# Kernel tuning notes

Measured on AMD Instinct MI355X. Metric: run time of the kernel, lower is better.

## Reference

```python
import jax, jax.numpy as jnp
import numpy as np

DECAY_EPS = 1e-8  # matches F.cosine_similarity eps
DECAY_RATE = 0.999  # buffer decay_rate


def setup_inputs() -> dict:
    key = jax.random.key(0)
    ks = jax.random.split(key, 6)
    B, M, D = 256, 65536, 1024
    return {
        "query": jax.random.normal(ks[0], (B, D), dtype=jnp.float32),
        "mem_keys": jax.random.normal(ks[1], (M, D), dtype=jnp.float32),
        "mem_values": jax.random.normal(ks[2], (M, D), dtype=jnp.float32),
        "importance": jax.random.uniform(ks[3], (M,), dtype=jnp.float32),
        "access_times": jax.random.randint(ks[4], (M,), 0, 1000, dtype=jnp.int32),
        "access_counts": jax.random.randint(ks[5], (M,), 1, 50, dtype=jnp.int32),
        "current_time": 1000,
        "top_k": 8,
    }


def reference(query, mem_keys, mem_values, importance, access_times, access_counts, current_time, top_k):
    # Batched version of AdaptiveMemoryBuffer.retrieve.
    # query: [B, D]; mem_keys/mem_values: [M, D]; importance/access_*: [M]
    qn = query / jnp.maximum(jnp.linalg.norm(query, axis=-1, keepdims=True), DECAY_EPS)
    kn = mem_keys / jnp.maximum(jnp.linalg.norm(mem_keys, axis=-1, keepdims=True), DECAY_EPS)
    sim = qn @ kn.T  # [B, M] cosine similarity

    dt = (current_time - access_times).astype(jnp.float32)           # time since access
    retention = jnp.power(jnp.float32(DECAY_RATE), dt)               # forgetting curve
    freq_bonus = jnp.log1p(access_counts.astype(jnp.float32))        # log(1 + count)
    scores = sim * (retention * importance * freq_bonus)[None, :]    # [B, M]

    top_scores, top_idx = jax.lax.top_k(scores, top_k)                # [B, k]
    weights = jax.nn.softmax(top_scores, axis=-1)                     # [B, k]
    combined = jnp.einsum('bk,bkd->bd', weights, mem_values[top_idx]) # weighted gather
    confidence = weights.max(axis=-1)                                 # [B]
    return combined, confidence
```

## Files before the change

kernel.cpp:

```cpp
#include <hip/hip_runtime.h>
#include <math.h>
#include <float.h>

typedef __attribute__((ext_vector_type(8))) short short8;
typedef __attribute__((ext_vector_type(8))) ushort ushort8;
typedef __attribute__((ext_vector_type(4))) float f32x4;

namespace {

constexpr int B = 256;
constexpr int M = 65536;
constexpr int D = 1024;
constexpr float DECAY_EPS = 1e-8f;
constexpr float DECAY_RATE = 0.999f;

constexpr int BN = 32;
constexpr int BK = 32;
constexpr int KSTEPS = D / BK;

constexpr int CHUNKS = 8;
constexpr int CHUNK = M / CHUNKS;
constexpr int NCAND = CHUNKS * 8;

__device__ inline ushort f2bf(float f) {
  union { float f; unsigned u; } v; v.f = f;
  unsigned r = v.u + 0x7fffu + ((v.u >> 16) & 1u);
  return (ushort)(r >> 16);
}

__global__ void prep_q_kernel(const float* __restrict__ q, ushort* __restrict__ qnf) {
  const int r = blockIdx.x;
  const int t = threadIdx.x;
  float4 v = reinterpret_cast<const float4*>(q + (size_t)r * D)[t];
  float ss = v.x * v.x + v.y * v.y + v.z * v.z + v.w * v.w;
#pragma unroll
  for (int off = 32; off; off >>= 1) ss += __shfl_down(ss, off, 64);
  __shared__ float red[4];
  if ((t & 63) == 0) red[t >> 6] = ss;
  __syncthreads();
  const float inv = 1.0f / fmaxf(sqrtf(red[0] + red[1] + red[2] + red[3]), DECAY_EPS);
  ushort4 o;
  o.x = f2bf(v.x * inv); o.y = f2bf(v.y * inv);
  o.z = f2bf(v.z * inv); o.w = f2bf(v.w * inv);
  const int k0 = t * 4;
  const int kt = k0 >> 5;
  const int lane_slot = (r & 15) + 16 * ((k0 & 31) >> 3);
  const int j0 = k0 & 7;
  *reinterpret_cast<ushort4*>(qnf + (size_t)(kt * 16 + (r >> 4)) * 512 + lane_slot * 8 + j0) = o;
}

__global__ __launch_bounds__(512, 8) void score_gemm_kernel(
    const ushort* __restrict__ qnf, const float* __restrict__ keys,
    const float* __restrict__ importance, const int* __restrict__ atimes,
    const int* __restrict__ acnts, const int* __restrict__ ctime,
    ushort* __restrict__ scores) {
  __shared__ alignas(16) ushort Bs[2][BN * BK];
  __shared__ float cscale[BN];

  const int t = threadIdx.x;
  const int lane = t & 63;
  const int w = t >> 6;
  const int h = lane >> 4;
  const int q = lane & 15;
  const int jb = blockIdx.x * BN;

  const int rw = t >> 4;
  const int cw = t & 15;
  const float2* kp2 = reinterpret_cast<const float2*>(keys + (size_t)(jb + rw) * D) + cw;
  const int wo = rw * BK + (((cw >> 2) ^ ((rw >> 1) & 3)) * 4 + (cw & 3)) * 2;

  int roff[2];
#pragma unroll
  for (int nf = 0; nf < 2; ++nf) {
    const int row = nf * 16 + q;
    roff[nf] = row * BK + ((h ^ ((row >> 1) & 3)) * 8);
  }

  f32x4 acc[2][2];
#pragma unroll
  for (int f = 0; f < 2; ++f)
#pragma unroll
    for (int n = 0; n < 2; ++n) acc[f][n] = (f32x4)(0.0f);

  float kn2 = 0.0f;
  float2 nv;

  nv = kp2[0];
  kn2 += nv.x * nv.x + nv.y * nv.y;
  *reinterpret_cast<uint*>(&Bs[0][wo]) = (uint)f2bf(nv.x) | ((uint)f2bf(nv.y) << 16);
  nv = kp2[16];
  __syncthreads();

  const short8* apbase = reinterpret_cast<const short8*>(qnf);

  for (int s = 0; s < KSTEPS; ++s) {
    const int cur = s & 1;
    short8 a0 = apbase[(size_t)(s * 16 + 2 * w + 0) * 64 + lane];
    short8 a1 = apbase[(size_t)(s * 16 + 2 * w + 1) * 64 + lane];
    short8 b0 = *reinterpret_cast<const short8*>(&Bs[cur][roff[0]]);
    short8 b1 = *reinterpret_cast<const short8*>(&Bs[cur][roff[1]]);
    acc[0][0] = __builtin_amdgcn_mfma_f32_16x16x32_bf16(a0, b0, acc[0][0], 0, 0, 0);
    acc[0][1] = __builtin_amdgcn_mfma_f32_16x16x32_bf16(a0, b1, acc[0][1], 0, 0, 0);
    acc[1][0] = __builtin_amdgcn_mfma_f32_16x16x32_bf16(a1, b0, acc[1][0], 0, 0, 0);
    acc[1][1] = __builtin_amdgcn_mfma_f32_16x16x32_bf16(a1, b1, acc[1][1], 0, 0, 0);
    if (s + 1 < KSTEPS) {
      kn2 += nv.x * nv.x + nv.y * nv.y;
      *reinterpret_cast<uint*>(&Bs[cur ^ 1][wo]) =
          (uint)f2bf(nv.x) | ((uint)f2bf(nv.y) << 16);
      if (s + 2 < KSTEPS) nv = kp2[(s + 2) * 16];
    }
    __syncthreads();
  }

  kn2 += __shfl_xor(kn2, 1, 64);
  kn2 += __shfl_xor(kn2, 2, 64);
  kn2 += __shfl_xor(kn2, 4, 64);
  kn2 += __shfl_xor(kn2, 8, 64);
  if (q == 0) {
    const int j = jb + rw;
    const float dt = (float)(ctime[0] - atimes[j]);
    const float mult = powf(DECAY_RATE, dt) * importance[j] * log1pf((float)acnts[j]);
    cscale[rw] = mult / fmaxf(sqrtf(kn2), DECAY_EPS);
  }
  __syncthreads();

#pragma unroll
  for (int f = 0; f < 2; ++f) {
    const int row0 = (2 * w + f) * 16 + (h << 2);
#pragma unroll
    for (int nf = 0; nf < 2; ++nf) {
      const float cs = cscale[nf * 16 + q];
#pragma unroll
      for (int rr = 0; rr < 4; ++rr) {
        const float v = acc[f][nf][rr] * cs;
        const float vn = __shfl_xor(v, 1, 64);
        if (!(q & 1)) {
          const uint pk = (uint)f2bf(v) | ((uint)f2bf(vn) << 16);
          *reinterpret_cast<uint*>(
              scores + (size_t)(row0 + rr) * M + jb + nf * 16 + q) = pk;
        }
      }
    }
  }
}

__global__ __launch_bounds__(256) void topk_partial_kernel(
    const ushort* __restrict__ scores, int* __restrict__ cand_i) {
  const int b = blockIdx.y;
  const int c = blockIdx.x;
  const int t = threadIdx.x;
  const int lane = t & 63, w = t >> 6;
  const ushort8* base8 =
      reinterpret_cast<const ushort8*>(scores + (size_t)b * M + (size_t)c * CHUNK);

  uint s8[8];
#pragma unroll
  for (int i = 0; i < 8; ++i) s8[i] = 0;

  auto ins = [&](uint x) {
    if (x > s8[0]) {
#pragma unroll
      for (int i = 0; i < 8; ++i) {
        const bool up = (i < 7) && (x > s8[i + 1]);
        const uint keep = (x > s8[i]) ? x : s8[i];
        s8[i] = up ? s8[i + 1] : keep;
      }
    }
  };

  const uint jbase = (uint)c * CHUNK;
#pragma unroll
  for (int it = 0; it < CHUNK / (256 * 8); ++it) {
    const int slot = it * 256 + t;
    const ushort8 v = base8[slot];
    const uint j0 = jbase + (uint)slot * 8;
#pragma unroll
    for (int e = 0; e < 8; ++e) {
      const ushort s = (ushort)v[e];
      const ushort key = (s & 0x8000) ? (ushort)~s : (ushort)(s | 0x8000);
      ins(((uint)key << 16) | ((j0 + e) & 0xFFFFu));
    }
  }

  __shared__ uint ls[2048];
#pragma unroll
  for (int i = 0; i < 8; ++i) ls[t * 8 + i] = s8[i];
  __syncthreads();

  __shared__ uint rs4[4];
  __shared__ int rp4[4];
  for (int r = 0; r < 8; ++r) {
    uint ms = 0;
    int mp = 0;
#pragma unroll
    for (int i = 0; i < 8; ++i) {
      const uint v = ls[i * 256 + t];
      if (v > ms) { ms = v; mp = i * 256 + t; }
    }
#pragma unroll
    for (int off = 32; off; off >>= 1) {
      const uint ov = __shfl_xor(ms, off, 64);
      const int op = __shfl_xor(mp, off, 64);
      if (ov > ms) { ms = ov; mp = op; }
    }
    if (lane == 0) { rs4[w] = ms; rp4[w] = mp; }
    __syncthreads();
    if (t == 0) {
      uint bs = 0;
      int bp = 0;
#pragma unroll
      for (int i = 0; i < 4; ++i)
        if (rs4[i] > bs) { bs = rs4[i]; bp = rp4[i]; }
      cand_i[((size_t)b * CHUNKS + c) * 8 + r] = (int)(ls[bp] & 0xFFFFu);
      ls[bp] = 0;
    }
    __syncthreads();
  }
}

__global__ __launch_bounds__(512) void rescore_kernel(
    const int* __restrict__ cand_i, const float* __restrict__ query,
    const float* __restrict__ keys, const float* __restrict__ values,
    const float* __restrict__ importance, const int* __restrict__ atimes,
    const int* __restrict__ acnts, const int* __restrict__ ctime,
    float* __restrict__ outc, float* __restrict__ conf) {
  const int b = blockIdx.x;
  const int t = threadIdx.x;
  const int lane = t & 63, w = t >> 6;

  const float4* qv4 = reinterpret_cast<const float4*>(query + (size_t)b * D + lane * 16);
  float4 q0 = qv4[0], q1 = qv4[1], q2 = qv4[2], q3 = qv4[3];
  float ssq = q0.x * q0.x + q0.y * q0.y + q0.z * q0.z + q0.w * q0.w
            + q1.x * q1.x + q1.y * q1.y + q1.z * q1.z + q1.w * q1.w
            + q2.x * q2.x + q2.y * q2.y + q2.z * q2.z + q2.w * q2.w
            + q3.x * q3.x + q3.y * q3.y + q3.z * q3.z + q3.w * q3.w;
#pragma unroll
  for (int off = 32; off; off >>= 1) ssq += __shfl_xor(ssq, off, 64);
  const float qdn = fmaxf(sqrtf(ssq), DECAY_EPS);
  const int ct = ctime[0];

  __shared__ float sc[NCAND];
  __shared__ int sidx[NCAND];

  for (int u = 0; u < 8; ++u) {
    const int c = w * 8 + u;
    const int j = cand_i[(size_t)b * NCAND + c];
    const float4* kv4 = reinterpret_cast<const float4*>(keys + (size_t)j * D + lane * 16);
    const float4 k0 = kv4[0], k1 = kv4[1], k2 = kv4[2], k3 = kv4[3];
    float dd = q0.x * k0.x + q0.y * k0.y + q0.z * k0.z + q0.w * k0.w
             + q1.x * k1.x + q1.y * k1.y + q1.z * k1.z + q1.w * k1.w
             + q2.x * k2.x + q2.y * k2.y + q2.z * k2.z + q2.w * k2.w
             + q3.x * k3.x + q3.y * k3.y + q3.z * k3.z + q3.w * k3.w;
    float nn = k0.x * k0.x + k0.y * k0.y + k0.z * k0.z + k0.w * k0.w
             + k1.x * k1.x + k1.y * k1.y + k1.z * k1.z + k1.w * k1.w
             + k2.x * k2.x + k2.y * k2.y + k2.z * k2.z + k2.w * k2.w
             + k3.x * k3.x + k3.y * k3.y + k3.z * k3.z + k3.w * k3.w;
#pragma unroll
    for (int off = 32; off; off >>= 1) {
      dd += __shfl_xor(dd, off, 64);
      nn += __shfl_xor(nn, off, 64);
    }
    if (lane == 0) {
      const float dtv = (float)(ct - atimes[j]);
      const float mult = powf(DECAY_RATE, dtv) * importance[j] * log1pf((float)acnts[j]);
      sc[c] = dd / (qdn * fmaxf(sqrtf(nn), DECAY_EPS)) * mult;
      sidx[c] = j;
    }
  }
  __syncthreads();

  __shared__ float w8s[8];
  __shared__ int g8[8];
  __shared__ float confv;
  __shared__ float tls[8];
  __shared__ int tli[8];
  if (w == 0) {
    float myv = sc[lane];
    for (int r = 0; r < 8; ++r) {
      float m = myv;
      int mi = lane;
#pragma unroll
      for (int off = 32; off; off >>= 1) {
        const float ov = __shfl_xor(m, off, 64);
        const int oi = __shfl_xor(mi, off, 64);
        if (ov > m || (ov == m && oi < mi)) { m = ov; mi = oi; }
      }
      if (lane == 0) { tls[r] = m; tli[r] = mi; }
      if (lane == mi) myv = -FLT_MAX;
    }
    if (lane == 0) {
      const float mx = tls[0];
      float e[8];
      float z = 0.0f;
#pragma unroll
      for (int r = 0; r < 8; ++r) { e[r] = expf(tls[r] - mx); z += e[r]; }
      const float invz = 1.0f / z;
#pragma unroll
      for (int r = 0; r < 8; ++r) { w8s[r] = e[r] * invz; g8[r] = sidx[tli[r]]; }
      confv = w8s[0];
    }
  }
  __syncthreads();

  float2 acc = make_float2(0.0f, 0.0f);
#pragma unroll
  for (int k = 0; k < 8; ++k) {
    const float wk = w8s[k];
    const float2 v = *reinterpret_cast<const float2*>(values + (size_t)g8[k] * D + 2 * t);
    acc.x = fmaf(wk, v.x, acc.x);
    acc.y = fmaf(wk, v.y, acc.y);
  }
  *reinterpret_cast<float2*>(outc + (size_t)b * D + 2 * t) = acc;
  if (t == 0) conf[b] = confv;
}

}

extern "C" void kernel_launch(void* const* d_in, const int* in_sizes, int n_in,
                              void* d_out, int out_size, void* d_ws, size_t ws_size,
                              hipStream_t stream) {
  const float* query = (const float*)d_in[0];
  const float* keys = (const float*)d_in[1];
  const float* values = (const float*)d_in[2];
  const float* importance = (const float*)d_in[3];
  const int* atimes = (const int*)d_in[4];
  const int* acnts = (const int*)d_in[5];
  const int* ctime = (const int*)d_in[6];

  float* out = (float*)d_out;
  ushort* qnf = (ushort*)d_ws;
  ushort* scores = qnf + (size_t)B * D;
  int* cand = (int*)(scores + (size_t)B * M);

  prep_q_kernel<<<B, 256, 0, stream>>>(query, qnf);
  score_gemm_kernel<<<M / BN, 512, 0, stream>>>(qnf, keys, importance, atimes,
                                                acnts, ctime, scores);
  dim3 gA(CHUNKS, B);
  topk_partial_kernel<<<gA, 256, 0, stream>>>(scores, cand);
  rescore_kernel<<<B, 512, 0, stream>>>(cand, query, keys, values, importance,
                                        atimes, acnts, ctime, out, out + (size_t)B * D);
}
```

Before: 163.6 us.

## Load key fragments directly into registers and drop LDS staging in score GEMM

```diff
diff --git a/kernel.cpp b/kernel.cpp
--- a/kernel.cpp
+++ b/kernel.cpp
@@ -1,4 +1,5 @@
 #include <hip/hip_runtime.h>
+#include <hip/hip_bf16.h>
 #include <math.h>
 #include <float.h>
 
@@ -15,8 +16,7 @@
 constexpr float DECAY_RATE = 0.999f;
 
 constexpr int BN = 32;
-constexpr int BK = 32;
-constexpr int KSTEPS = D / BK;
+constexpr int KSTEPS = D / 32;
 
 constexpr int CHUNKS = 8;
 constexpr int CHUNK = M / CHUNKS;
@@ -26,6 +26,22 @@
   union { float f; unsigned u; } v; v.f = f;
   unsigned r = v.u + 0x7fffu + ((v.u >> 16) & 1u);
   return (ushort)(r >> 16);
+}
+
+__device__ inline short bfs(float f) {
+  __hip_bfloat16 h = __float2bfloat16(f);
+  return *reinterpret_cast<const short*>(&h);
+}
+
+__device__ inline short8 pack8(float4 u, float4 v) {
+  short8 r;
+  r[0] = bfs(u.x); r[1] = bfs(u.y); r[2] = bfs(u.z); r[3] = bfs(u.w);
+  r[4] = bfs(v.x); r[5] = bfs(v.y); r[6] = bfs(v.z); r[7] = bfs(v.w);
+  return r;
+}
+
+__device__ inline float dot4(float4 a) {
+  return a.x * a.x + a.y * a.y + a.z * a.z + a.w * a.w;
 }
 
 __global__ void prep_q_kernel(const float* __restrict__ q, ushort* __restrict__ qnf) {
@@ -49,14 +65,11 @@
   *reinterpret_cast<ushort4*>(qnf + (size_t)(kt * 16 + (r >> 4)) * 512 + lane_slot * 8 + j0) = o;
 }
 
-__global__ __launch_bounds__(512, 8) void score_gemm_kernel(
+__global__ __launch_bounds__(256) void score_gemm_kernel(
     const ushort* __restrict__ qnf, const float* __restrict__ keys,
     const float* __restrict__ importance, const int* __restrict__ atimes,
     const int* __restrict__ acnts, const int* __restrict__ ctime,
     ushort* __restrict__ scores) {
-  __shared__ alignas(16) ushort Bs[2][BN * BK];
-  __shared__ float cscale[BN];
-
   const int t = threadIdx.x;
   const int lane = t & 63;
   const int w = t >> 6;
@@ -64,75 +77,77 @@
   const int q = lane & 15;
   const int jb = blockIdx.x * BN;
 
-  const int rw = t >> 4;
-  const int cw = t & 15;
-  const float2* kp2 = reinterpret_cast<const float2*>(keys + (size_t)(jb + rw) * D) + cw;
-  const int wo = rw * BK + (((cw >> 2) ^ ((rw >> 1) & 3)) * 4 + (cw & 3)) * 2;
-
-  int roff[2];
-#pragma unroll
-  for (int nf = 0; nf < 2; ++nf) {
-    const int row = nf * 16 + q;
-    roff[nf] = row * BK + ((h ^ ((row >> 1) & 3)) * 8);
-  }
-
-  f32x4 acc[2][2];
-#pragma unroll
-  for (int f = 0; f < 2; ++f)
+  const float* kb0 = keys + (size_t)(jb + q) * D + h * 8;
+  const float* kb1 = keys + (size_t)(jb + 16 + q) * D + h * 8;
+  const short8* ap = reinterpret_cast<const short8*>(qnf) + (size_t)(w * 4) * 64 + lane;
+
+  f32x4 acc[4][2];
+#pragma unroll
+  for (int f = 0; f < 4; ++f)
 #pragma unroll
     for (int n = 0; n < 2; ++n) acc[f][n] = (f32x4)(0.0f);
 
-  float kn2 = 0.0f;
-  float2 nv;
-
-  nv = kp2[0];
-  kn2 += nv.x * nv.x + nv.y * nv.y;
-  *reinterpret_cast<uint*>(&Bs[0][wo]) = (uint)f2bf(nv.x) | ((uint)f2bf(nv.y) << 16);
-  nv = kp2[16];
-  __syncthreads();
-
-  const short8* apbase = reinterpret_cast<const short8*>(qnf);
-
-  for (int s = 0; s < KSTEPS; ++s) {
-    const int cur = s & 1;
-    short8 a0 = apbase[(size_t)(s * 16 + 2 * w + 0) * 64 + lane];
-    short8 a1 = apbase[(size_t)(s * 16 + 2 * w + 1) * 64 + lane];
-    short8 b0 = *reinterpret_cast<const short8*>(&Bs[cur][roff[0]]);
-    short8 b1 = *reinterpret_cast<const short8*>(&Bs[cur][roff[1]]);
-    acc[0][0] = __builtin_amdgcn_mfma_f32_16x16x32_bf16(a0, b0, acc[0][0], 0, 0, 0);
-    acc[0][1] = __builtin_amdgcn_mfma_f32_16x16x32_bf16(a0, b1, acc[0][1], 0, 0, 0);
-    acc[1][0] = __builtin_amdgcn_mfma_f32_16x16x32_bf16(a1, b0, acc[1][0], 0, 0, 0);
-    acc[1][1] = __builtin_amdgcn_mfma_f32_16x16x32_bf16(a1, b1, acc[1][1], 0, 0, 0);
-    if (s + 1 < KSTEPS) {
-      kn2 += nv.x * nv.x + nv.y * nv.y;
-      *reinterpret_cast<uint*>(&Bs[cur ^ 1][wo]) =
-          (uint)f2bf(nv.x) | ((uint)f2bf(nv.y) << 16);
-      if (s + 2 < KSTEPS) nv = kp2[(s + 2) * 16];
-    }
-    __syncthreads();
-  }
-
-  kn2 += __shfl_xor(kn2, 1, 64);
-  kn2 += __shfl_xor(kn2, 2, 64);
-  kn2 += __shfl_xor(kn2, 4, 64);
-  kn2 += __shfl_xor(kn2, 8, 64);
-  if (q == 0) {
-    const int j = jb + rw;
-    const float dt = (float)(ctime[0] - atimes[j]);
-    const float mult = powf(DECAY_RATE, dt) * importance[j] * log1pf((float)acnts[j]);
-    cscale[rw] = mult / fmaxf(sqrtf(kn2), DECAY_EPS);
-  }
-  __syncthreads();
-
-#pragma unroll
-  for (int f = 0; f < 2; ++f) {
-    const int row0 = (2 * w + f) * 16 + (h << 2);
+  float kn0 = 0.0f, kn1 = 0.0f;
+
+  short8 aA[4], aB[4];
+  float4 bA[4], bB[4];
+
+  auto LA = [&](short8* aa, int s) {
+#pragma unroll
+    for (int f = 0; f < 4; ++f) aa[f] = ap[(size_t)(s * 16 + f) * 64];
+  };
+  auto LB = [&](float4* bb, int s) {
+    bb[0] = *reinterpret_cast<const float4*>(kb0 + s * 32);
+    bb[1] = *reinterpret_cast<const float4*>(kb0 + s * 32 + 4);
+    bb[2] = *reinterpret_cast<const float4*>(kb1 + s * 32);
+    bb[3] = *reinterpret_cast<const float4*>(kb1 + s * 32 + 4);
+  };
+  auto CMP = [&](short8* aa, float4* bb) {
+    kn0 += dot4(bb[0]) + dot4(bb[1]);
+    kn1 += dot4(bb[2]) + dot4(bb[3]);
+    const short8 b0 = pack8(bb[0], bb[1]);
+    const short8 b1 = pack8(bb[2], bb[3]);
+#pragma unroll
+    for (int f = 0; f < 4; ++f) {
+      acc[f][0] = __builtin_amdgcn_mfma_f32_16x16x32_bf16(aa[f], b0, acc[f][0], 0, 0, 0);
+      acc[f][1] = __builtin_amdgcn_mfma_f32_16x16x32_bf16(aa[f], b1, acc[f][1], 0, 0, 0);
+    }
+  };
+
+  LA(aA, 0); LB(bA, 0);
+  for (int it = 0; it < KSTEPS / 2; ++it) {
+    LA(aB, 2 * it + 1); LB(bB, 2 * it + 1);
+    CMP(aA, bA);
+    if (it < KSTEPS / 2 - 1) { LA(aA, 2 * it + 2); LB(bA, 2 * it + 2); }
+    CMP(aB, bB);
+  }
+
+  kn0 += __shfl_xor(kn0, 16, 64); kn0 += __shfl_xor(kn0, 32, 64);
+  kn1 += __shfl_xor(kn1, 16, 64); kn1 += __shfl_xor(kn1, 32, 64);
+
+  const int ct = ctime[0];
+  float cs[2];
+  {
+    const int j = jb + q;
+    const float mult = powf(DECAY_RATE, (float)(ct - atimes[j])) * importance[j] *
+                       log1pf((float)acnts[j]);
+    cs[0] = mult / fmaxf(sqrtf(kn0), DECAY_EPS);
+  }
+  {
+    const int j = jb + 16 + q;
+    const float mult = powf(DECAY_RATE, (float)(ct - atimes[j])) * importance[j] *
+                       log1pf((float)acnts[j]);
+    cs[1] = mult / fmaxf(sqrtf(kn1), DECAY_EPS);
+  }
+
+#pragma unroll
+  for (int f = 0; f < 4; ++f) {
+    const int row0 = (w * 4 + f) * 16 + (h << 2);
 #pragma unroll
     for (int nf = 0; nf < 2; ++nf) {
-      const float cs = cscale[nf * 16 + q];
 #pragma unroll
       for (int rr = 0; rr < 4; ++rr) {
-        const float v = acc[f][nf][rr] * cs;
+        const float v = acc[f][nf][rr] * cs[nf];
         const float vn = __shfl_xor(v, 1, 64);
         if (!(q & 1)) {
           const uint pk = (uint)f2bf(v) | ((uint)f2bf(vn) << 16);
@@ -230,10 +245,7 @@
 
   const float4* qv4 = reinterpret_cast<const float4*>(query + (size_t)b * D + lane * 16);
   float4 q0 = qv4[0], q1 = qv4[1], q2 = qv4[2], q3 = qv4[3];
-  float ssq = q0.x * q0.x + q0.y * q0.y + q0.z * q0.z + q0.w * q0.w
-            + q1.x * q1.x + q1.y * q1.y + q1.z * q1.z + q1.w * q1.w
-            + q2.x * q2.x + q2.y * q2.y + q2.z * q2.z + q2.w * q2.w
-            + q3.x * q3.x + q3.y * q3.y + q3.z * q3.z + q3.w * q3.w;
+  float ssq = dot4(q0) + dot4(q1) + dot4(q2) + dot4(q3);
 #pragma unroll
   for (int off = 32; off; off >>= 1) ssq += __shfl_xor(ssq, off, 64);
   const float qdn = fmaxf(sqrtf(ssq), DECAY_EPS);
@@ -251,10 +263,7 @@
              + q1.x * k1.x + q1.y * k1.y + q1.z * k1.z + q1.w * k1.w
              + q2.x * k2.x + q2.y * k2.y + q2.z * k2.z + q2.w * k2.w
              + q3.x * k3.x + q3.y * k3.y + q3.z * k3.z + q3.w * k3.w;
-    float nn = k0.x * k0.x + k0.y * k0.y + k0.z * k0.z + k0.w * k0.w
-             + k1.x * k1.x + k1.y * k1.y + k1.z * k1.z + k1.w * k1.w
-             + k2.x * k2.x + k2.y * k2.y + k2.z * k2.z + k2.w * k2.w
-             + k3.x * k3.x + k3.y * k3.y + k3.z * k3.z + k3.w * k3.w;
+    float nn = dot4(k0) + dot4(k1) + dot4(k2) + dot4(k3);
 #pragma unroll
     for (int off = 32; off; off >>= 1) {
       dd += __shfl_xor(dd, off, 64);
@@ -333,7 +342,7 @@
   int* cand = (int*)(scores + (size_t)B * M);
 
   prep_q_kernel<<<B, 256, 0, stream>>>(query, qnf);
-  score_gemm_kernel<<<M / BN, 512, 0, stream>>>(qnf, keys, importance, atimes,
+  score_gemm_kernel<<<M / BN, 256, 0, stream>>>(qnf, keys, importance, atimes,
                                                 acnts, ctime, scores);
   dim3 gA(CHUNKS, B);
   topk_partial_kernel<<<gA, 256, 0, stream>>>(scores, cand);
```

Result: slower. 219.4 us (+34.1%).

## Enlarge score GEMM tile to 64 keys with 4x4 MFMA per wave

Applied to the files above, without the earlier changes.

```diff
diff --git a/kernel.cpp b/kernel.cpp
--- a/kernel.cpp
+++ b/kernel.cpp
@@ -14,7 +14,7 @@
 constexpr float DECAY_EPS = 1e-8f;
 constexpr float DECAY_RATE = 0.999f;
 
-constexpr int BN = 32;
+constexpr int BN = 64;
 constexpr int BK = 32;
 constexpr int KSTEPS = D / BK;
 
@@ -28,11 +28,24 @@
   return (ushort)(r >> 16);
 }
 
+__device__ inline short8 pack8(float4 u, float4 v) {
+  short8 r;
+  r[0] = (short)f2bf(u.x); r[1] = (short)f2bf(u.y);
+  r[2] = (short)f2bf(u.z); r[3] = (short)f2bf(u.w);
+  r[4] = (short)f2bf(v.x); r[5] = (short)f2bf(v.y);
+  r[6] = (short)f2bf(v.z); r[7] = (short)f2bf(v.w);
+  return r;
+}
+
+__device__ inline float dot4(float4 a) {
+  return a.x * a.x + a.y * a.y + a.z * a.z + a.w * a.w;
+}
+
 __global__ void prep_q_kernel(const float* __restrict__ q, ushort* __restrict__ qnf) {
   const int r = blockIdx.x;
   const int t = threadIdx.x;
   float4 v = reinterpret_cast<const float4*>(q + (size_t)r * D)[t];
-  float ss = v.x * v.x + v.y * v.y + v.z * v.z + v.w * v.w;
+  float ss = dot4(v);
 #pragma unroll
   for (int off = 32; off; off >>= 1) ss += __shfl_down(ss, off, 64);
   __shared__ float red[4];
@@ -49,7 +62,7 @@
   *reinterpret_cast<ushort4*>(qnf + (size_t)(kt * 16 + (r >> 4)) * 512 + lane_slot * 8 + j0) = o;
 }
 
-__global__ __launch_bounds__(512, 8) void score_gemm_kernel(
+__global__ __launch_bounds__(256, 4) void score_gemm_kernel(
     const ushort* __restrict__ qnf, const float* __restrict__ keys,
     const float* __restrict__ importance, const int* __restrict__ atimes,
     const int* __restrict__ acnts, const int* __restrict__ ctime,
@@ -64,59 +77,84 @@
   const int q = lane & 15;
   const int jb = blockIdx.x * BN;
 
-  const int rw = t >> 4;
-  const int cw = t & 15;
-  const float2* kp2 = reinterpret_cast<const float2*>(keys + (size_t)(jb + rw) * D) + cw;
-  const int wo = rw * BK + (((cw >> 2) ^ ((rw >> 1) & 3)) * 4 + (cw & 3)) * 2;
-
-  int roff[2];
-#pragma unroll
-  for (int nf = 0; nf < 2; ++nf) {
+  const int rw = t >> 2;
+  const int cw = t & 3;
+  const float* kptr = keys + (size_t)(jb + rw) * D + cw * 8;
+  const int wo = rw * BK + ((cw ^ ((rw >> 1) & 3)) * 8);
+
+  int roff[4];
+#pragma unroll
+  for (int nf = 0; nf < 4; ++nf) {
     const int row = nf * 16 + q;
     roff[nf] = row * BK + ((h ^ ((row >> 1) & 3)) * 8);
   }
 
-  f32x4 acc[2][2];
-#pragma unroll
-  for (int f = 0; f < 2; ++f)
-#pragma unroll
-    for (int n = 0; n < 2; ++n) acc[f][n] = (f32x4)(0.0f);
+  f32x4 acc[4][4];
+#pragma unroll
+  for (int f = 0; f < 4; ++f)
+#pragma unroll
+    for (int n = 0; n < 4; ++n) acc[f][n] = (f32x4)(0.0f);
 
   float kn2 = 0.0f;
-  float2 nv;
-
-  nv = kp2[0];
-  kn2 += nv.x * nv.x + nv.y * nv.y;
-  *reinterpret_cast<uint*>(&Bs[0][wo]) = (uint)f2bf(nv.x) | ((uint)f2bf(nv.y) << 16);
-  nv = kp2[16];
-  __syncthreads();
-
-  const short8* apbase = reinterpret_cast<const short8*>(qnf);
-
+
+  {
+    float4 v0 = *reinterpret_cast<const float4*>(kptr);
+    float4 v1 = *reinterpret_cast<const float4*>(kptr + 4);
+    kn2 += dot4(v0) + dot4(v1);
+    *reinterpret_cast<short8*>(&Bs[0][wo]) = pack8(v0, v1);
+  }
+  float4 nvA0 = *reinterpret_cast<const float4*>(kptr + 1 * BK);
+  float4 nvA1 = *reinterpret_cast<const float4*>(kptr + 1 * BK + 4);
+  float4 nvB0 = *reinterpret_cast<const float4*>(kptr + 2 * BK);
+  float4 nvB1 = *reinterpret_cast<const float4*>(kptr + 2 * BK + 4);
+  asm volatile("s_waitcnt lgkmcnt(0)" ::: "memory");
+  __builtin_amdgcn_s_barrier();
+
+  const short8* ap = reinterpret_cast<const short8*>(qnf) + (size_t)(w * 4) * 64 + lane;
+
+#pragma unroll
   for (int s = 0; s < KSTEPS; ++s) {
     const int cur = s & 1;
-    short8 a0 = apbase[(size_t)(s * 16 + 2 * w + 0) * 64 + lane];
-    short8 a1 = apbase[(size_t)(s * 16 + 2 * w + 1) * 64 + lane];
+    short8 a0 = ap[(size_t)(s * 16 + 0) * 64];
+    short8 a1 = ap[(size_t)(s * 16 + 1) * 64];
+    short8 a2 = ap[(size_t)(s * 16 + 2) * 64];
+    short8 a3 = ap[(size_t)(s * 16 + 3) * 64];
+    if (s < KSTEPS - 1) {
+      float4 u0 = (s & 1) ? nvB0 : nvA0;
+      float4 u1 = (s & 1) ? nvB1 : nvA1;
+      kn2 += dot4(u0) + dot4(u1);
+      *reinterpret_cast<short8*>(&Bs[cur ^ 1][wo]) = pack8(u0, u1);
+    }
+    if (s < KSTEPS - 3) {
+      if (s & 1) {
+        nvB0 = *reinterpret_cast<const float4*>(kptr + (s + 3) * BK);
+        nvB1 = *reinterpret_cast<const float4*>(kptr + (s + 3) * BK + 4);
+      } else {
+        nvA0 = *reinterpret_cast<const float4*>(kptr + (s + 3) * BK);
+        nvA1 = *reinterpret_cast<const float4*>(kptr + (s + 3) * BK + 4);
+      }
+    }
     short8 b0 = *reinterpret_cast<const short8*>(&Bs[cur][roff[0]]);
     short8 b1 = *reinterpret_cast<const short8*>(&Bs[cur][roff[1]]);
-    acc[0][0] = __builtin_amdgcn_mfma_f32_16x16x32_bf16(a0, b0, acc[0][0], 0, 0, 0);
-    acc[0][1] = __builtin_amdgcn_mfma_f32_16x16x32_bf16(a0, b1, acc[0][1], 0, 0, 0);
-    acc[1][0] = __builtin_amdgcn_mfma_f32_16x16x32_bf16(a1, b0, acc[1][0], 0, 0, 0);
-    acc[1][1] = __builtin_amdgcn_mfma_f32_16x16x32_bf16(a1, b1, acc[1][1], 0, 0, 0);
-    if (s + 1 < KSTEPS) {
-      kn2 += nv.x * nv.x + nv.y * nv.y;
-      *reinterpret_cast<uint*>(&Bs[cur ^ 1][wo]) =
-          (uint)f2bf(nv.x) | ((uint)f2bf(nv.y) << 16);
-      if (s + 2 < KSTEPS) nv = kp2[(s + 2) * 16];
-    }
-    __syncthreads();
+    short8 b2 = *reinterpret_cast<const short8*>(&Bs[cur][roff[2]]);
+    short8 b3 = *reinterpret_cast<const short8*>(&Bs[cur][roff[3]]);
+#pragma unroll
+    for (int f = 0; f < 4; ++f) {
+      const short8 af = (f == 0) ? a0 : (f == 1) ? a1 : (f == 2) ? a2 : a3;
+      acc[f][0] = __builtin_amdgcn_mfma_f32_16x16x32_bf16(af, b0, acc[f][0], 0, 0, 0);
+      acc[f][1] = __builtin_amdgcn_mfma_f32_16x16x32_bf16(af, b1, acc[f][1], 0, 0, 0);
+      acc[f][2] = __builtin_amdgcn_mfma_f32_16x16x32_bf16(af, b2, acc[f][2], 0, 0, 0);
+      acc[f][3] = __builtin_amdgcn_mfma_f32_16x16x32_bf16(af, b3, acc[f][3], 0, 0, 0);
+    }
+    if (s < KSTEPS - 1) {
+      asm volatile("s_waitcnt lgkmcnt(0)" ::: "memory");
+      __builtin_amdgcn_s_barrier();
+    }
   }
 
   kn2 += __shfl_xor(kn2, 1, 64);
   kn2 += __shfl_xor(kn2, 2, 64);
-  kn2 += __shfl_xor(kn2, 4, 64);
-  kn2 += __shfl_xor(kn2, 8, 64);
-  if (q == 0) {
+  if (cw == 0) {
     const int j = jb + rw;
     const float dt = (float)(ctime[0] - atimes[j]);
     const float mult = powf(DECAY_RATE, dt) * importance[j] * log1pf((float)acnts[j]);
@@ -124,15 +162,17 @@
   }
   __syncthreads();
 
-#pragma unroll
-  for (int f = 0; f < 2; ++f) {
-    const int row0 = (2 * w + f) * 16 + (h << 2);
-#pragma unroll
-    for (int nf = 0; nf < 2; ++nf) {
-      const float cs = cscale[nf * 16 + q];
+  float cs[4];
+#pragma unroll
+  for (int nf = 0; nf < 4; ++nf) cs[nf] = cscale[nf * 16 + q];
+#pragma unroll
+  for (int f = 0; f < 4; ++f) {
+    const int row0 = (w * 4 + f) * 16 + (h << 2);
+#pragma unroll
+    for (int nf = 0; nf < 4; ++nf) {
 #pragma unroll
       for (int rr = 0; rr < 4; ++rr) {
-        const float v = acc[f][nf][rr] * cs;
+        const float v = acc[f][nf][rr] * cs[nf];
         const float vn = __shfl_xor(v, 1, 64);
         if (!(q & 1)) {
           const uint pk = (uint)f2bf(v) | ((uint)f2bf(vn) << 16);
@@ -230,10 +270,7 @@
 
   const float4* qv4 = reinterpret_cast<const float4*>(query + (size_t)b * D + lane * 16);
   float4 q0 = qv4[0], q1 = qv4[1], q2 = qv4[2], q3 = qv4[3];
-  float ssq = q0.x * q0.x + q0.y * q0.y + q0.z * q0.z + q0.w * q0.w
-            + q1.x * q1.x + q1.y * q1.y + q1.z * q1.z + q1.w * q1.w
-            + q2.x * q2.x + q2.y * q2.y + q2.z * q2.z + q2.w * q2.w
-            + q3.x * q3.x + q3.y * q3.y + q3.z * q3.z + q3.w * q3.w;
+  float ssq = dot4(q0) + dot4(q1) + dot4(q2) + dot4(q3);
 #pragma unroll
   for (int off = 32; off; off >>= 1) ssq += __shfl_xor(ssq, off, 64);
   const float qdn = fmaxf(sqrtf(ssq), DECAY_EPS);
@@ -251,10 +288,7 @@
              + q1.x * k1.x + q1.y * k1.y + q1.z * k1.z + q1.w * k1.w
              + q2.x * k2.x + q2.y * k2.y + q2.z * k2.z + q2.w * k2.w
              + q3.x * k3.x + q3.y * k3.y + q3.z * k3.z + q3.w * k3.w;
-    float nn = k0.x * k0.x + k0.y * k0.y + k0.z * k0.z + k0.w * k0.w
-             + k1.x * k1.x + k1.y * k1.y + k1.z * k1.z + k1.w * k1.w
-             + k2.x * k2.x + k2.y * k2.y + k2.z * k2.z + k2.w * k2.w
-             + k3.x * k3.x + k3.y * k3.y + k3.z * k3.z + k3.w * k3.w;
+    float nn = dot4(k0) + dot4(k1) + dot4(k2) + dot4(k3);
 #pragma unroll
     for (int off = 32; off; off >>= 1) {
       dd += __shfl_xor(dd, off, 64);
@@ -333,7 +367,7 @@
   int* cand = (int*)(scores + (size_t)B * M);
 
   prep_q_kernel<<<B, 256, 0, stream>>>(query, qnf);
-  score_gemm_kernel<<<M / BN, 512, 0, stream>>>(qnf, keys, importance, atimes,
+  score_gemm_kernel<<<M / BN, 256, 0, stream>>>(qnf, keys, importance, atimes,
                                                 acnts, ctime, scores);
   dim3 gA(CHUNKS, B);
   topk_partial_kernel<<<gA, 256, 0, stream>>>(scores, cand);
```

Result: slower. 332.8 us (+103.4%).
